# Optimization experiments

Hardware: AMD Instinct MI355X
Metric: run time of the kernel (lower is better)

Reference implementation:

```python
import jax, jax.numpy as jnp
import numpy as np

H = 32       # num query heads
KV = 8       # num kv heads
HD = 128     # head dim
G = H // KV  # groups


def setup_inputs() -> dict:
    key = jax.random.key(0)
    ks = jax.random.split(key, 7)
    B, S, P, D = 2, 2048, 1024, 4096
    s = 1.0 / np.sqrt(D)
    return {
        "x": jax.random.normal(ks[0], (B, S, D), jnp.float32),
        "past_k": jax.random.normal(ks[1], (B, P, KV, HD), jnp.float32),
        "past_v": jax.random.normal(ks[2], (B, P, KV, HD), jnp.float32),
        "Wq": jax.random.normal(ks[3], (D, H * HD), jnp.float32) * s,
        "Wk": jax.random.normal(ks[4], (D, KV * HD), jnp.float32) * s,
        "Wv": jax.random.normal(ks[5], (D, KV * HD), jnp.float32) * s,
        "Wo": jax.random.normal(ks[6], (D, D), jnp.float32) * s,
    }


def reference(x, past_k, past_v, Wq, Wk, Wv, Wo):
    B, S, D = x.shape
    q = (x @ Wq).reshape(B, S, H, HD)    # [B,S,H,hd]
    k = (x @ Wk).reshape(B, S, KV, HD)
    v = (x @ Wv).reshape(B, S, KV, HD)
    # KV-cache append (cache slice [:, :end])
    k_full = jnp.concatenate([past_k, k], axis=1)  # [B,T,KV,hd]
    v_full = jnp.concatenate([past_v, v], axis=1)
    T = k_full.shape[1]
    # repeat_interleave over head dim -> each kv head serves G query heads
    k_rep = jnp.repeat(k_full, G, axis=2)  # [B,T,H,hd]
    v_rep = jnp.repeat(v_full, G, axis=2)
    scale = 1.0 / np.sqrt(HD)
    scores = jnp.einsum('bshd,bthd->bhst', q, k_rep) * scale  # [B,H,S,T]
    # causal mask with cache offset: query i attends to j <= (T - S) + i
    allowed = (jnp.arange(S)[:, None] + (T - S)) >= jnp.arange(T)[None, :]
    scores = jnp.where(allowed[None, None], scores, jnp.float32(-jnp.inf))
    attn = jax.nn.softmax(scores, axis=-1)
    out = jnp.einsum('bhst,bthd->bshd', attn, v_rep).reshape(B, S, D)
    return out @ Wo
```

## Files before the change

kernel.cpp:

```cpp
#include <hip/hip_runtime.h>

typedef __bf16 bf16x8 __attribute__((ext_vector_type(8)));
typedef float f32x4 __attribute__((ext_vector_type(4)));

#define B_ 2
#define S_ 2048
#define D_ 4096
#define H_ 32
#define KV_ 8
#define G_ 4
#define HD_ 128
#define P_ 1024
#define T_ 3072

__device__ inline bf16x8 cvt8(const float4 a, const float4 b) {
  bf16x8 r;
  r[0] = (__bf16)a.x; r[1] = (__bf16)a.y; r[2] = (__bf16)a.z; r[3] = (__bf16)a.w;
  r[4] = (__bf16)b.x; r[5] = (__bf16)b.y; r[6] = (__bf16)b.z; r[7] = (__bf16)b.w;
  return r;
}

__global__ __launch_bounds__(256) void cvt_f32_bf16(const float* __restrict__ in,
                                                    __bf16* __restrict__ out) {
  const long i = ((long)blockIdx.x * 256 + threadIdx.x) * 8;
  float4 a = *(const float4*)(in + i);
  float4 b = *(const float4*)(in + i + 4);
  *(bf16x8*)(out + i) = cvt8(a, b);
}

__global__ __launch_bounds__(256) void transpose2d(const float* __restrict__ in,
                                                   __bf16* __restrict__ out,
                                                   int R, int C) {
  __shared__ float tl[32][33];
  const int tx = threadIdx.x, ty = threadIdx.y;
  const int c0 = blockIdx.x * 32, r0 = blockIdx.y * 32;
#pragma unroll
  for (int i = 0; i < 4; ++i)
    tl[ty + i * 8][tx] = in[(long)(r0 + ty + i * 8) * C + c0 + tx];
  __syncthreads();
#pragma unroll
  for (int i = 0; i < 4; ++i)
    out[(long)(c0 + ty + i * 8) * R + r0 + tx] = (__bf16)tl[tx][ty + i * 8];
}

__global__ __launch_bounds__(256) void build_vt(const float* __restrict__ past_v,
                                                const __bf16* __restrict__ vn,
                                                __bf16* __restrict__ vt) {
  __shared__ float tl[32][33];
  const int tx = threadIdx.x, ty = threadIdx.y;
  const int j0 = blockIdx.x * 32, hd0 = blockIdx.y * 32;
  const int b = blockIdx.z >> 3, kvh = blockIdx.z & 7;
#pragma unroll
  for (int i = 0; i < 4; ++i) {
    const int j = j0 + ty + i * 8;
    float val = (j < P_)
        ? past_v[((long)((b * P_ + j) * KV_ + kvh)) * HD_ + hd0 + tx]
        : (float)vn[((long)((b * S_ + (j - P_)) * KV_ + kvh)) * HD_ + hd0 + tx];
    tl[ty + i * 8][tx] = val;
  }
  __syncthreads();
#pragma unroll
  for (int i = 0; i < 4; ++i)
    vt[((long)((b * KV_ + kvh) * HD_ + hd0 + ty + i * 8)) * T_ + j0 + tx] =
        (__bf16)tl[tx][ty + i * 8];
}

template <typename OutT>
__global__ __launch_bounds__(256, 2) void gemm_bt(const __bf16* __restrict__ A,
                                                  const __bf16* __restrict__ Bt,
                                                  OutT* __restrict__ C,
                                                  int M, int N, int K) {
  __shared__ __align__(16) __bf16 As[128][40];
  __shared__ __align__(16) __bf16 Bs[128][40];
  const int t = threadIdx.x;
  const int lane = t & 63, wave = t >> 6;
  const int wm = (wave >> 1) * 64, wn = (wave & 1) * 64;
  const int l15 = lane & 15, quad = lane >> 4;
  const long m0 = (long)blockIdx.y * 128, n0 = (long)blockIdx.x * 128;

  const int srow = t >> 2;
  const int sc8 = (t & 3) * 8;
  const __bf16* Ap = A + (m0 + srow) * K + sc8;
  const __bf16* Bp = Bt + (n0 + srow) * K + sc8;
  const long rstep = (long)64 * K;

  f32x4 acc[4][4];
#pragma unroll
  for (int i = 0; i < 4; ++i)
#pragma unroll
    for (int j = 0; j < 4; ++j)
#pragma unroll
      for (int e = 0; e < 4; ++e) acc[i][j][e] = 0.0f;

  bf16x8 ra0 = *(const bf16x8*)(Ap);
  bf16x8 ra1 = *(const bf16x8*)(Ap + rstep);
  bf16x8 rb0 = *(const bf16x8*)(Bp);
  bf16x8 rb1 = *(const bf16x8*)(Bp + rstep);

  const int nk = K >> 5;
  for (int kt = 0; kt < nk; ++kt) {
    __syncthreads();
    *(bf16x8*)(&As[srow][sc8]) = ra0;
    *(bf16x8*)(&As[64 + srow][sc8]) = ra1;
    *(bf16x8*)(&Bs[srow][sc8]) = rb0;
    *(bf16x8*)(&Bs[64 + srow][sc8]) = rb1;
    if (kt + 1 < nk) {
      const __bf16* An = Ap + (kt + 1) * 32;
      const __bf16* Bn = Bp + (kt + 1) * 32;
      ra0 = *(const bf16x8*)(An);
      ra1 = *(const bf16x8*)(An + rstep);
      rb0 = *(const bf16x8*)(Bn);
      rb1 = *(const bf16x8*)(Bn + rstep);
    }
    __syncthreads();
    bf16x8 aF[4], bF[4];
#pragma unroll
    for (int i = 0; i < 4; ++i)
      aF[i] = *(const bf16x8*)(&As[wm + i * 16 + l15][quad * 8]);
#pragma unroll
    for (int i = 0; i < 4; ++i)
      bF[i] = *(const bf16x8*)(&Bs[wn + i * 16 + l15][quad * 8]);
#pragma unroll
    for (int i = 0; i < 4; ++i)
#pragma unroll
      for (int j = 0; j < 4; ++j)
        acc[i][j] = __builtin_amdgcn_mfma_f32_16x16x32_bf16(aF[i], bF[j],
                                                            acc[i][j], 0, 0, 0);
  }

#pragma unroll
  for (int i = 0; i < 4; ++i) {
    const long r0 = m0 + wm + i * 16 + quad * 4;
#pragma unroll
    for (int j = 0; j < 4; ++j) {
      const long col = n0 + wn + j * 16 + l15;
#pragma unroll
      for (int r = 0; r < 4; ++r)
        C[(r0 + r) * N + col] = (OutT)acc[i][j][r];
    }
  }
}

__global__ __launch_bounds__(256, 2) void attn_kernel(
    __bf16* qio,
    const float* __restrict__ pk,
    const __bf16* __restrict__ kn,
    const __bf16* __restrict__ vt) {
  __shared__ __align__(16) __bf16 Ks[32][136];
  __shared__ __align__(16) __bf16 Vs[128][40];
  __shared__ __align__(16) __bf16 Ps[4][16][40];
  const int t = threadIdx.x;
  const int lane = t & 63, w = t >> 6;
  const int l15 = lane & 15, quad = lane >> 4;
  const int s0 = blockIdx.x * 64;
  const int h = blockIdx.y;
  const int b = blockIdx.z;
  const int kvh = h >> 2;

  bf16x8 aQ[4];
  {
    const int qrow = s0 + w * 16 + l15;
    const __bf16* qp = qio + ((long)((b * S_ + qrow) * H_ + h)) * HD_ + quad * 8;
#pragma unroll
    for (int kt = 0; kt < 4; ++kt) aQ[kt] = *(const bf16x8*)(qp + kt * 32);
  }

  f32x4 O[8];
#pragma unroll
  for (int f = 0; f < 8; ++f)
#pragma unroll
    for (int e = 0; e < 4; ++e) O[f][e] = 0.0f;
  float m_r[4], l_r[4];
#pragma unroll
  for (int r = 0; r < 4; ++r) { m_r[r] = -__builtin_inff(); l_r[r] = 0.0f; }

  const float C2 = 1.4426950408889634f * 0.08838834764831845f;
  const int ntiles = (P_ + s0 + 63) / 32 + 1;

  for (int tile = 0; tile < ntiles; ++tile) {
    const int j0 = tile * 32;
    __syncthreads();
#pragma unroll
    for (int p = 0; p < 2; ++p) {
      const int li = p * 256 + t;
      const int key = li >> 4, ch = (li & 15) * 8;
      const int j = j0 + key;
      bf16x8 kv;
      if (j < P_) {
        const float* src = pk + ((long)((b * P_ + j) * KV_ + kvh)) * HD_ + ch;
        kv = cvt8(*(const float4*)src, *(const float4*)(src + 4));
      } else {
        kv = *(const bf16x8*)(kn + ((long)((b * S_ + (j - P_)) * KV_ + kvh)) * HD_ + ch);
      }
      *(bf16x8*)(&Ks[key][ch]) = kv;
    }
#pragma unroll
    for (int p = 0; p < 2; ++p) {
      const int li = p * 256 + t;
      const int hd = li >> 2, k8 = (li & 3) * 8;
      *(bf16x8*)(&Vs[hd][k8]) =
          *(const bf16x8*)(vt + ((long)((b * KV_ + kvh) * HD_ + hd)) * T_ + j0 + k8);
    }
    __syncthreads();

    f32x4 sc0, sc1;
#pragma unroll
    for (int e = 0; e < 4; ++e) { sc0[e] = 0.0f; sc1[e] = 0.0f; }
#pragma unroll
    for (int kt = 0; kt < 4; ++kt) {
      bf16x8 bk0 = *(const bf16x8*)(&Ks[l15][kt * 32 + quad * 8]);
      bf16x8 bk1 = *(const bf16x8*)(&Ks[16 + l15][kt * 32 + quad * 8]);
      sc0 = __builtin_amdgcn_mfma_f32_16x16x32_bf16(aQ[kt], bk0, sc0, 0, 0, 0);
      sc1 = __builtin_amdgcn_mfma_f32_16x16x32_bf16(aQ[kt], bk1, sc1, 0, 0, 0);
    }

    float alpha[4];
#pragma unroll
    for (int r = 0; r < 4; ++r) {
      const int bound = P_ + s0 + w * 16 + quad * 4 + r;
      float v0 = (j0 + l15 <= bound) ? sc0[r] : -__builtin_inff();
      float v1 = (j0 + 16 + l15 <= bound) ? sc1[r] : -__builtin_inff();
      float mt = fmaxf(v0, v1);
      mt = fmaxf(mt, __shfl_xor(mt, 1));
      mt = fmaxf(mt, __shfl_xor(mt, 2));
      mt = fmaxf(mt, __shfl_xor(mt, 4));
      mt = fmaxf(mt, __shfl_xor(mt, 8));
      const float mn = fmaxf(m_r[r], mt);
      const float p0 = exp2f((v0 - mn) * C2);
      const float p1 = exp2f((v1 - mn) * C2);
      float rs = p0 + p1;
      rs += __shfl_xor(rs, 1);
      rs += __shfl_xor(rs, 2);
      rs += __shfl_xor(rs, 4);
      rs += __shfl_xor(rs, 8);
      alpha[r] = exp2f((m_r[r] - mn) * C2);
      m_r[r] = mn;
      l_r[r] = l_r[r] * alpha[r] + rs;
      Ps[w][quad * 4 + r][l15] = (__bf16)p0;
      Ps[w][quad * 4 + r][16 + l15] = (__bf16)p1;
    }
#pragma unroll
    for (int f = 0; f < 8; ++f)
#pragma unroll
      for (int r = 0; r < 4; ++r) O[f][r] *= alpha[r];

    __syncthreads();

    bf16x8 aP = *(const bf16x8*)(&Ps[w][l15][quad * 8]);
#pragma unroll
    for (int f = 0; f < 8; ++f) {
      bf16x8 bV = *(const bf16x8*)(&Vs[f * 16 + l15][quad * 8]);
      O[f] = __builtin_amdgcn_mfma_f32_16x16x32_bf16(aP, bV, O[f], 0, 0, 0);
    }
  }

#pragma unroll
  for (int r = 0; r < 4; ++r) {
    const float inv = 1.0f / l_r[r];
    const long row = (long)((b * S_ + s0 + w * 16 + quad * 4 + r) * H_ + h);
#pragma unroll
    for (int f = 0; f < 8; ++f)
      qio[row * HD_ + f * 16 + l15] = (__bf16)(O[f][r] * inv);
  }
}

extern "C" void kernel_launch(void* const* d_in, const int* in_sizes, int n_in,
                              void* d_out, int out_size, void* d_ws, size_t ws_size,
                              hipStream_t stream) {
  const float* x  = (const float*)d_in[0];
  const float* pk = (const float*)d_in[1];
  const float* pv = (const float*)d_in[2];
  const float* Wq = (const float*)d_in[3];
  const float* Wk = (const float*)d_in[4];
  const float* Wv = (const float*)d_in[5];
  const float* Wo = (const float*)d_in[6];
  float* out = (float*)d_out;
  char* ws = (char*)d_ws;
  __bf16* wt = (__bf16*)(ws);
  __bf16* q  = (__bf16*)(ws + (size_t)33554432);
  __bf16* kn = (__bf16*)(ws + (size_t)67108864);
  __bf16* vn = (__bf16*)(ws + (size_t)75497472);
  __bf16* xb = (__bf16*)(ws + (size_t)83886080);
  __bf16* vt = (__bf16*)(ws + (size_t)83886080);

  dim3 tb(32, 8);
  cvt_f32_bf16<<<8192, 256, 0, stream>>>(x, xb);
  transpose2d<<<dim3(128, 128), tb, 0, stream>>>(Wq, wt, D_, D_);
  gemm_bt<__bf16><<<dim3(32, 32), 256, 0, stream>>>(xb, wt, q, B_ * S_, D_, D_);
  transpose2d<<<dim3(32, 128), tb, 0, stream>>>(Wk, wt, D_, KV_ * HD_);
  gemm_bt<__bf16><<<dim3(8, 32), 256, 0, stream>>>(xb, wt, kn, B_ * S_, KV_ * HD_, D_);
  transpose2d<<<dim3(32, 128), tb, 0, stream>>>(Wv, wt, D_, KV_ * HD_);
  gemm_bt<__bf16><<<dim3(8, 32), 256, 0, stream>>>(xb, wt, vn, B_ * S_, KV_ * HD_, D_);
  build_vt<<<dim3(96, 4, 16), tb, 0, stream>>>(pv, vn, vt);
  attn_kernel<<<dim3(32, 32, 2), 256, 0, stream>>>(q, pk, kn, vt);
  transpose2d<<<dim3(128, 128), tb, 0, stream>>>(Wo, wt, D_, D_);
  gemm_bt<float><<<dim3(32, 32), 256, 0, stream>>>(q, wt, out, B_ * S_, D_, D_);
}
```

Before: 1.309 ms.

## Restructure attention with 256-row query blocks, pre-packed bf16 K cache, heavy-first ordering

A new kernel packs past_k and the new K into a contiguous bf16 [B,KV,T,HD] buffer, so the attention loop no longer converts fp32 on the fly. The attention kernel now uses 512 threads covering 256 query rows, with two 16-row fragments per wave and 64-key tiles. This gives more reuse of each K/V tile held in LDS and fewer barriers per key. The score fragment is computed transposed, which cuts the shuffle reductions. Masking is applied only on diagonal tiles, waves skip tiles past their causal limit, and blocks are launched heaviest-first. The cost is an extra packing kernel and much more LDS and register use per block, which may lower occupancy.

```diff
diff --git a/kernel.cpp b/kernel.cpp
--- a/kernel.cpp
+++ b/kernel.cpp
@@ -1,6 +1,7 @@
 #include <hip/hip_runtime.h>
 
 typedef __bf16 bf16x8 __attribute__((ext_vector_type(8)));
+typedef __bf16 bf16x4 __attribute__((ext_vector_type(4)));
 typedef float f32x4 __attribute__((ext_vector_type(4)));
 
 #define B_ 2
@@ -63,6 +64,24 @@
   for (int i = 0; i < 4; ++i)
     vt[((long)((b * KV_ + kvh) * HD_ + hd0 + ty + i * 8)) * T_ + j0 + tx] =
         (__bf16)tl[tx][ty + i * 8];
+}
+
+__global__ __launch_bounds__(256) void build_kc(const float* __restrict__ pk,
+                                                const __bf16* __restrict__ kn,
+                                                __bf16* __restrict__ kc) {
+  const int idx = blockIdx.x * 256 + threadIdx.x;
+  const int row = idx >> 4, ch = (idx & 15) * 8;
+  const int j = row % T_;
+  const int kvq = row / T_;
+  const int kvh = kvq % KV_, b = kvq / KV_;
+  bf16x8 vv;
+  if (j < P_) {
+    const float* src = pk + ((long)((b * P_ + j) * KV_ + kvh)) * HD_ + ch;
+    vv = cvt8(*(const float4*)src, *(const float4*)(src + 4));
+  } else {
+    vv = *(const bf16x8*)(kn + ((long)((b * S_ + (j - P_)) * KV_ + kvh)) * HD_ + ch);
+  }
+  *(bf16x8*)(kc + (long)row * HD_ + ch) = vv;
 }
 
 template <typename OutT>
@@ -141,126 +160,160 @@
   }
 }
 
-__global__ __launch_bounds__(256, 2) void attn_kernel(
+__global__ __launch_bounds__(512, 4) void attn_kernel(
     __bf16* qio,
-    const float* __restrict__ pk,
-    const __bf16* __restrict__ kn,
+    const __bf16* __restrict__ kc,
     const __bf16* __restrict__ vt) {
-  __shared__ __align__(16) __bf16 Ks[32][136];
-  __shared__ __align__(16) __bf16 Vs[128][40];
-  __shared__ __align__(16) __bf16 Ps[4][16][40];
+  __shared__ __align__(16) __bf16 Ks[64][136];
+  __shared__ __align__(16) __bf16 Vs[128][72];
+  __shared__ __align__(16) __bf16 Ps[256][72];
   const int t = threadIdx.x;
   const int lane = t & 63, w = t >> 6;
   const int l15 = lane & 15, quad = lane >> 4;
-  const int s0 = blockIdx.x * 64;
-  const int h = blockIdx.y;
-  const int b = blockIdx.z;
+  const int s0 = (7 - (int)blockIdx.x) * 256;
+  const int h = blockIdx.y, b = blockIdx.z;
   const int kvh = h >> 2;
-
-  bf16x8 aQ[4];
-  {
-    const int qrow = s0 + w * 16 + l15;
+  const long kcb = (long)(b * KV_ + kvh) * T_;
+  const long vtb = (long)(b * KV_ + kvh) * HD_;
+
+  bf16x8 aQ[2][4];
+#pragma unroll
+  for (int mi = 0; mi < 2; ++mi) {
+    const int qrow = s0 + w * 32 + mi * 16 + l15;
     const __bf16* qp = qio + ((long)((b * S_ + qrow) * H_ + h)) * HD_ + quad * 8;
 #pragma unroll
-    for (int kt = 0; kt < 4; ++kt) aQ[kt] = *(const bf16x8*)(qp + kt * 32);
-  }
-
-  f32x4 O[8];
-#pragma unroll
-  for (int f = 0; f < 8; ++f)
-#pragma unroll
-    for (int e = 0; e < 4; ++e) O[f][e] = 0.0f;
-  float m_r[4], l_r[4];
-#pragma unroll
-  for (int r = 0; r < 4; ++r) { m_r[r] = -__builtin_inff(); l_r[r] = 0.0f; }
+    for (int kt = 0; kt < 4; ++kt) aQ[mi][kt] = *(const bf16x8*)(qp + kt * 32);
+  }
+
+  f32x4 O[2][8];
+#pragma unroll
+  for (int mi = 0; mi < 2; ++mi)
+#pragma unroll
+    for (int f = 0; f < 8; ++f)
+#pragma unroll
+      for (int e = 0; e < 4; ++e) O[mi][f][e] = 0.0f;
+  float m_r[2] = {-__builtin_inff(), -__builtin_inff()};
+  float l_r[2] = {0.0f, 0.0f};
 
   const float C2 = 1.4426950408889634f * 0.08838834764831845f;
-  const int ntiles = (P_ + s0 + 63) / 32 + 1;
+  const int ntiles = (P_ + s0 + 256) / 64;
+  const int wave_last_key = P_ + s0 + w * 32 + 31;
+  const int wave_min_bound = P_ + s0 + w * 32;
 
   for (int tile = 0; tile < ntiles; ++tile) {
-    const int j0 = tile * 32;
+    const int j0 = tile * 64;
     __syncthreads();
 #pragma unroll
     for (int p = 0; p < 2; ++p) {
-      const int li = p * 256 + t;
+      const int li = p * 512 + t;
       const int key = li >> 4, ch = (li & 15) * 8;
-      const int j = j0 + key;
-      bf16x8 kv;
-      if (j < P_) {
-        const float* src = pk + ((long)((b * P_ + j) * KV_ + kvh)) * HD_ + ch;
-        kv = cvt8(*(const float4*)src, *(const float4*)(src + 4));
-      } else {
-        kv = *(const bf16x8*)(kn + ((long)((b * S_ + (j - P_)) * KV_ + kvh)) * HD_ + ch);
+      *(bf16x8*)(&Ks[key][ch]) =
+          *(const bf16x8*)(kc + (kcb + j0 + key) * HD_ + ch);
+    }
+#pragma unroll
+    for (int p = 0; p < 2; ++p) {
+      const int li = p * 512 + t;
+      const int hd = li >> 3, k8 = (li & 7) * 8;
+      *(bf16x8*)(&Vs[hd][k8]) =
+          *(const bf16x8*)(vt + (vtb + hd) * T_ + j0 + k8);
+    }
+    __syncthreads();
+
+    if (j0 > wave_last_key) continue;
+
+    const bool need_mask = (j0 + 63 > wave_min_bound);
+    float alpha_l[2];
+
+#pragma unroll
+    for (int mi = 0; mi < 2; ++mi) {
+      f32x4 sc[4];
+#pragma unroll
+      for (int kf = 0; kf < 4; ++kf)
+#pragma unroll
+        for (int e = 0; e < 4; ++e) sc[kf][e] = 0.0f;
+#pragma unroll
+      for (int kf = 0; kf < 4; ++kf)
+#pragma unroll
+        for (int kt = 0; kt < 4; ++kt) {
+          bf16x8 bk = *(const bf16x8*)(&Ks[kf * 16 + l15][kt * 32 + quad * 8]);
+          sc[kf] = __builtin_amdgcn_mfma_f32_16x16x32_bf16(bk, aQ[mi][kt],
+                                                           sc[kf], 0, 0, 0);
+        }
+      const int boundq = P_ + s0 + w * 32 + mi * 16 + l15;
+      float v[4][4];
+      float mloc = -__builtin_inff();
+#pragma unroll
+      for (int kf = 0; kf < 4; ++kf) {
+        const int kb = j0 + kf * 16 + quad * 4;
+#pragma unroll
+        for (int r = 0; r < 4; ++r) {
+          float x = sc[kf][r];
+          if (need_mask && (kb + r > boundq)) x = -__builtin_inff();
+          v[kf][r] = x;
+          mloc = fmaxf(mloc, x);
+        }
       }
-      *(bf16x8*)(&Ks[key][ch]) = kv;
-    }
-#pragma unroll
-    for (int p = 0; p < 2; ++p) {
-      const int li = p * 256 + t;
-      const int hd = li >> 2, k8 = (li & 3) * 8;
-      *(bf16x8*)(&Vs[hd][k8]) =
-          *(const bf16x8*)(vt + ((long)((b * KV_ + kvh) * HD_ + hd)) * T_ + j0 + k8);
-    }
-    __syncthreads();
-
-    f32x4 sc0, sc1;
-#pragma unroll
-    for (int e = 0; e < 4; ++e) { sc0[e] = 0.0f; sc1[e] = 0.0f; }
-#pragma unroll
-    for (int kt = 0; kt < 4; ++kt) {
-      bf16x8 bk0 = *(const bf16x8*)(&Ks[l15][kt * 32 + quad * 8]);
-      bf16x8 bk1 = *(const bf16x8*)(&Ks[16 + l15][kt * 32 + quad * 8]);
-      sc0 = __builtin_amdgcn_mfma_f32_16x16x32_bf16(aQ[kt], bk0, sc0, 0, 0, 0);
-      sc1 = __builtin_amdgcn_mfma_f32_16x16x32_bf16(aQ[kt], bk1, sc1, 0, 0, 0);
-    }
-
-    float alpha[4];
+      float mt = fmaxf(mloc, __shfl_xor(mloc, 16));
+      mt = fmaxf(mt, __shfl_xor(mt, 32));
+      const float mn = fmaxf(m_r[mi], mt);
+      const float al = exp2f((m_r[mi] - mn) * C2);
+      m_r[mi] = mn;
+      float sloc = 0.0f;
+      const int prow = w * 32 + mi * 16 + l15;
+#pragma unroll
+      for (int kf = 0; kf < 4; ++kf) {
+        const float p0 = exp2f((v[kf][0] - mn) * C2);
+        const float p1 = exp2f((v[kf][1] - mn) * C2);
+        const float p2 = exp2f((v[kf][2] - mn) * C2);
+        const float p3 = exp2f((v[kf][3] - mn) * C2);
+        sloc += (p0 + p1) + (p2 + p3);
+        bf16x4 pq;
+        pq[0] = (__bf16)p0; pq[1] = (__bf16)p1;
+        pq[2] = (__bf16)p2; pq[3] = (__bf16)p3;
+        *(bf16x4*)(&Ps[prow][kf * 16 + quad * 4]) = pq;
+      }
+      float rs = sloc + __shfl_xor(sloc, 16);
+      rs += __shfl_xor(rs, 32);
+      l_r[mi] = l_r[mi] * al + rs;
+      alpha_l[mi] = al;
+    }
+
+#pragma unroll
+    for (int mi = 0; mi < 2; ++mi)
+#pragma unroll
+      for (int r = 0; r < 4; ++r) {
+        const float aO = __shfl(alpha_l[mi], quad * 4 + r);
+#pragma unroll
+        for (int f = 0; f < 8; ++f) O[mi][f][r] *= aO;
+      }
+
+    __asm__ volatile("s_waitcnt lgkmcnt(0)" ::: "memory");
+
+#pragma unroll
+    for (int kf2 = 0; kf2 < 2; ++kf2) {
+      bf16x8 aP0 = *(const bf16x8*)(&Ps[w * 32 + l15][kf2 * 32 + quad * 8]);
+      bf16x8 aP1 = *(const bf16x8*)(&Ps[w * 32 + 16 + l15][kf2 * 32 + quad * 8]);
+#pragma unroll
+      for (int f = 0; f < 8; ++f) {
+        bf16x8 bV = *(const bf16x8*)(&Vs[f * 16 + l15][kf2 * 32 + quad * 8]);
+        O[0][f] = __builtin_amdgcn_mfma_f32_16x16x32_bf16(aP0, bV, O[0][f], 0, 0, 0);
+        O[1][f] = __builtin_amdgcn_mfma_f32_16x16x32_bf16(aP1, bV, O[1][f], 0, 0, 0);
+      }
+    }
+  }
+
+#pragma unroll
+  for (int mi = 0; mi < 2; ++mi) {
+    const float inv = 1.0f / l_r[mi];
 #pragma unroll
     for (int r = 0; r < 4; ++r) {
-      const int bound = P_ + s0 + w * 16 + quad * 4 + r;
-      float v0 = (j0 + l15 <= bound) ? sc0[r] : -__builtin_inff();
-      float v1 = (j0 + 16 + l15 <= bound) ? sc1[r] : -__builtin_inff();
-      float mt = fmaxf(v0, v1);
-      mt = fmaxf(mt, __shfl_xor(mt, 1));
-      mt = fmaxf(mt, __shfl_xor(mt, 2));
-      mt = fmaxf(mt, __shfl_xor(mt, 4));
-      mt = fmaxf(mt, __shfl_xor(mt, 8));
-      const float mn = fmaxf(m_r[r], mt);
-      const float p0 = exp2f((v0 - mn) * C2);
-      const float p1 = exp2f((v1 - mn) * C2);
-      float rs = p0 + p1;
-      rs += __shfl_xor(rs, 1);
-      rs += __shfl_xor(rs, 2);
-      rs += __shfl_xor(rs, 4);
-      rs += __shfl_xor(rs, 8);
-      alpha[r] = exp2f((m_r[r] - mn) * C2);
-      m_r[r] = mn;
-      l_r[r] = l_r[r] * alpha[r] + rs;
-      Ps[w][quad * 4 + r][l15] = (__bf16)p0;
-      Ps[w][quad * 4 + r][16 + l15] = (__bf16)p1;
-    }
-#pragma unroll
-    for (int f = 0; f < 8; ++f)
-#pragma unroll
-      for (int r = 0; r < 4; ++r) O[f][r] *= alpha[r];
-
-    __syncthreads();
-
-    bf16x8 aP = *(const bf16x8*)(&Ps[w][l15][quad * 8]);
-#pragma unroll
-    for (int f = 0; f < 8; ++f) {
-      bf16x8 bV = *(const bf16x8*)(&Vs[f * 16 + l15][quad * 8]);
-      O[f] = __builtin_amdgcn_mfma_f32_16x16x32_bf16(aP, bV, O[f], 0, 0, 0);
-    }
-  }
-
-#pragma unroll
-  for (int r = 0; r < 4; ++r) {
-    const float inv = 1.0f / l_r[r];
-    const long row = (long)((b * S_ + s0 + w * 16 + quad * 4 + r) * H_ + h);
-#pragma unroll
-    for (int f = 0; f < 8; ++f)
-      qio[row * HD_ + f * 16 + l15] = (__bf16)(O[f][r] * inv);
+      const float invr = __shfl(inv, quad * 4 + r);
+      const long row =
+          (long)((b * S_ + s0 + w * 32 + mi * 16 + quad * 4 + r) * H_ + h);
+#pragma unroll
+      for (int f = 0; f < 8; ++f)
+        qio[row * HD_ + f * 16 + l15] = (__bf16)(O[mi][f][r] * invr);
+    }
   }
 }
 
@@ -277,6 +330,7 @@
   float* out = (float*)d_out;
   char* ws = (char*)d_ws;
   __bf16* wt = (__bf16*)(ws);
+  __bf16* kc = (__bf16*)(ws);
   __bf16* q  = (__bf16*)(ws + (size_t)33554432);
   __bf16* kn = (__bf16*)(ws + (size_t)67108864);
   __bf16* vn = (__bf16*)(ws + (size_t)75497472);
@@ -292,7 +346,8 @@
   transpose2d<<<dim3(32, 128), tb, 0, stream>>>(Wv, wt, D_, KV_ * HD_);
   gemm_bt<__bf16><<<dim3(8, 32), 256, 0, stream>>>(xb, wt, vn, B_ * S_, KV_ * HD_, D_);
   build_vt<<<dim3(96, 4, 16), tb, 0, stream>>>(pv, vn, vt);
-  attn_kernel<<<dim3(32, 32, 2), 256, 0, stream>>>(q, pk, kn, vt);
+  build_kc<<<3072, 256, 0, stream>>>(pk, kn, kc);
+  attn_kernel<<<dim3(8, 32, 2), 512, 0, stream>>>(q, kc, vt);
   transpose2d<<<dim3(128, 128), tb, 0, stream>>>(Wo, wt, D_, D_);
   gemm_bt<float><<<dim3(32, 32), 256, 0, stream>>>(q, wt, out, B_ * S_, D_, D_);
 }
```

New measurement: 1.417 ms. +8.3%, slower.
